# Kernel optimization log

Measured on AMD Instinct MI355X. Metric: run time of the kernel, lower is better.

Reference implementation:

```python
import jax, jax.numpy as jnp
import numpy as np

B, NQ, ISIZE = 8, 2048, 1024
H, D, NA = 8, 128, 8            # num_head, attn_dim, num_anchor
AH = H * D                      # ahsize = 1024
ASZ = NA * D                    # anchor_size = 1024
FH = 4096                       # _fhsize
ISZ_NET = FH * H // NA          # 4096, input dim of self.net
EPS = 1e-6


def setup_inputs() -> dict:
    key = jax.random.key(0)
    ks = jax.random.split(key, 12)
    def u(k, shape, fan_in):
        s = 1.0 / np.sqrt(fan_in)
        return jax.random.uniform(k, shape, jnp.float32, -s, s)
    return {
        "inputs": jax.random.normal(ks[0], (B, NQ, ISIZE), jnp.float32),
        "ln_g": jnp.ones((ISIZE,), jnp.float32),
        "ln_b": jnp.zeros((ISIZE,), jnp.float32),
        "q_anchor": u(ks[1], (H, NA, D), D),
        "W_qkv": u(ks[2], (ISIZE, 3 * AH), ISIZE), "b_qkv": jnp.zeros((3 * AH,), jnp.float32),
        "W_an": u(ks[3], (ASZ, FH), ASZ), "b_an": jnp.zeros((FH,), jnp.float32),
        "W_n1": u(ks[4], (ISZ_NET, AH), ISZ_NET), "b_n1": jnp.zeros((AH,), jnp.float32),
        "W_n2": u(ks[5], (AH, FH), AH), "b_n2": jnp.zeros((FH,), jnp.float32),
        "W_n3": u(ks[6], (FH, AH), FH), "b_n3": jnp.zeros((AH,), jnp.float32),
        "W_k": u(ks[7], (AH, AH), AH), "b_k": jnp.zeros((AH,), jnp.float32),
        "W_o": u(ks[8], (AH, ISIZE), AH), "b_o": jnp.zeros((ISIZE,), jnp.float32),
    }


def reference(inputs, ln_g, ln_b, q_anchor, W_qkv, b_qkv, W_an, b_an,
              W_n1, b_n1, W_n2, b_n2, W_n3, b_n3, W_k, b_k, W_o, b_o):
    b, nq = inputs.shape[:2]
    scale = 1.0 / np.sqrt(D)
    # pre-LayerNorm
    mu = jnp.mean(inputs, -1, keepdims=True)
    var = jnp.mean(jnp.square(inputs - mu), -1, keepdims=True)
    x = (inputs - mu) * jax.lax.rsqrt(var + EPS) * ln_g + ln_b
    # QKV projection
    qkv = (x @ W_qkv + b_qkv).reshape(b, nq, 3, H, D)
    q = jnp.transpose(qkv[:, :, 0], (0, 2, 1, 3))   # [b,H,nq,D]
    k = qkv[:, :, 1]                                  # [b,nq,H,D]
    v = qkv[:, :, 2]                                  # [b,nq,H,D]
    # stage 1: fixed anchors attend over the sequence
    sc1 = jax.nn.softmax(jnp.einsum('had,bnhd->bhan', q_anchor, k) * scale, axis=-1)
    out = jnp.einsum('bhan,bnhd->bhad', sc1, v).reshape(b, H, ASZ)   # [b,H,NA*D]
    # anchor_net (share_head Linear + ReLU)
    out = jax.nn.relu(out @ W_an + b_an)                              # [b,H,FH]
    # regroup head-major -> anchor-major
    out = out.reshape(b, H, NA, FH // NA).transpose(0, 2, 1, 3).reshape(b, NA, ISZ_NET)
    # net: bottleneck Linear -> Linear -> ReLU -> Linear
    out = jax.nn.relu((out @ W_n1 + b_n1) @ W_n2 + b_n2) @ W_n3 + b_n3  # [b,NA,AH]
    # stage 2: queries attend over anchors
    kk = (out @ W_k + b_k).reshape(b, NA, H, D)
    sc2 = jax.nn.softmax(jnp.einsum('bhqd,bahd->bhqa', q, kk) * scale, axis=-1)
    ov = out.reshape(b, NA, H, D)
    y = jnp.einsum('bhqa,bahd->bqhd', sc2, ov).reshape(b, nq, AH)
    return y @ W_o + b_o + inputs
```

## Files before the change

### kernel.cpp

```cpp
#include <hip/hip_runtime.h>
#include <cstdint>
#include <cstddef>

typedef unsigned short u16;
typedef __attribute__((ext_vector_type(8))) short short8;
typedef __attribute__((ext_vector_type(4))) float floatx4;
typedef __attribute__((ext_vector_type(16))) float floatx16;

__device__ __forceinline__ u16 f2bf(float f) {
  unsigned u = __float_as_uint(f);
  u += 0x7fffu + ((u >> 16) & 1u);
  return (u16)(u >> 16);
}
__device__ __forceinline__ float bf2f(u16 s) {
  return __uint_as_float(((unsigned)s) << 16);
}

__global__ __launch_bounds__(256) void ln_kernel(const float* __restrict__ x,
                                                 const float* __restrict__ g,
                                                 const float* __restrict__ bta,
                                                 u16* __restrict__ out) {
  const int row = blockIdx.x;
  const int tid = threadIdx.x;
  const float4 v = ((const float4*)(x + (size_t)row * 1024))[tid];
  float s = v.x + v.y + v.z + v.w;
#pragma unroll
  for (int o = 32; o > 0; o >>= 1) s += __shfl_down(s, o);
  __shared__ float red[4], red2[4];
  const int wv = tid >> 6, ln = tid & 63;
  if (ln == 0) red[wv] = s;
  __syncthreads();
  const float mean = (red[0] + red[1] + red[2] + red[3]) * (1.0f / 1024.0f);
  const float dx = v.x - mean, dy = v.y - mean, dz = v.z - mean, dw = v.w - mean;
  float s2 = dx * dx + dy * dy + dz * dz + dw * dw;
#pragma unroll
  for (int o = 32; o > 0; o >>= 1) s2 += __shfl_down(s2, o);
  if (ln == 0) red2[wv] = s2;
  __syncthreads();
  const float var = (red2[0] + red2[1] + red2[2] + red2[3]) * (1.0f / 1024.0f);
  const float rstd = rsqrtf(var + 1e-6f);
  const float4 gg = ((const float4*)g)[tid];
  const float4 bb = ((const float4*)bta)[tid];
  ushort4 o4;
  o4.x = f2bf(dx * rstd * gg.x + bb.x);
  o4.y = f2bf(dy * rstd * gg.y + bb.y);
  o4.z = f2bf(dz * rstd * gg.z + bb.z);
  o4.w = f2bf(dw * rstd * gg.w + bb.w);
  ((ushort4*)(out + (size_t)row * 1024))[tid] = o4;
}

__global__ __launch_bounds__(256) void transpose2_bf16(const float* __restrict__ Wq,
                                                       u16* __restrict__ WqT,
                                                       const float* __restrict__ Wo,
                                                       u16* __restrict__ WoT) {
  __shared__ float t[32][33];
  const float* W;
  u16* WT;
  int N, yb;
  if (blockIdx.y < 96) { W = Wq; WT = WqT; N = 3072; yb = blockIdx.y; }
  else { W = Wo; WT = WoT; N = 1024; yb = blockIdx.y - 96; }
  const int kb = blockIdx.x * 32, nb = yb * 32;
  const int tx = threadIdx.x & 31, ty = threadIdx.x >> 5;
#pragma unroll
  for (int i = ty; i < 32; i += 8) t[i][tx] = W[(size_t)(kb + i) * N + nb + tx];
  __syncthreads();
#pragma unroll
  for (int i = ty; i < 32; i += 8) WT[(size_t)(nb + i) * 1024 + kb + tx] = f2bf(t[tx][i]);
}

__global__ __launch_bounds__(256) void init_bufs(const float* __restrict__ b_an,
                                                 const float* __restrict__ b_n1,
                                                 const float* __restrict__ b_n2,
                                                 const float* __restrict__ b_n3,
                                                 const float* __restrict__ b_k,
                                                 float* __restrict__ att1,
                                                 float* __restrict__ anp,
                                                 float* __restrict__ h1,
                                                 float* __restrict__ h2,
                                                 float* __restrict__ onet,
                                                 float* __restrict__ kkb) {
  const int i = blockIdx.x * 256 + threadIdx.x;
  if (i < 16384) {
    float4 z; z.x = 0.f; z.y = 0.f; z.z = 0.f; z.w = 0.f;
    ((float4*)att1)[i] = z;
  } else if (i < 81920) {
    const int j = i - 16384;
    ((float4*)anp)[j] = ((const float4*)b_an)[j & 1023];
  } else if (i < 98304) {
    const int j = i - 81920;
    ((float4*)h1)[j] = ((const float4*)b_n1)[j & 255];
  } else if (i < 163840) {
    const int j = i - 98304;
    ((float4*)h2)[j] = ((const float4*)b_n2)[j & 1023];
  } else if (i < 180224) {
    const int j = i - 163840;
    ((float4*)onet)[j] = ((const float4*)b_n3)[j & 255];
  } else {
    const int j = i - 180224;
    ((float4*)kkb)[j] = ((const float4*)b_k)[j & 255];
  }
}


__device__ __forceinline__ void stageG(const u16* __restrict__ gp, u16* lp, int K) {
  __builtin_amdgcn_global_load_lds((const __attribute__((address_space(1))) void*)gp,
                                   (__attribute__((address_space(3))) void*)lp, 16, 0, 0);
  __builtin_amdgcn_global_load_lds((const __attribute__((address_space(1))) void*)(gp + ((size_t)K << 6)),
                                   (__attribute__((address_space(3))) void*)(lp + 4096), 16, 0, 0);
}

__device__ __forceinline__ void rdA(short8 (&af)[2][4], const u16* sbuf, const int (&ab)[4],
                                    int halfoff) {
#pragma unroll
  for (int mi = 0; mi < 2; ++mi)
#pragma unroll
    for (int ks = 0; ks < 4; ++ks)
      af[mi][ks] = *(const short8*)(sbuf + halfoff + mi * 2048 + (ab[ks] ^ (mi << 5)));
}
__device__ __forceinline__ void rdB(short8 (&bf)[4], const u16* sbuf, const int (&bb)[4],
                                    int halfoff) {
#pragma unroll
  for (int ks = 0; ks < 4; ++ks)
    bf[ks] = *(const short8*)(sbuf + halfoff + bb[ks]);
}

template <int Q>
__device__ __forceinline__ void mfmaQ(floatx16 (&acc)[4][2], const short8 (&af)[2][4],
                                      const short8 (&bf)[4]) {
#pragma unroll
  for (int ks = 0; ks < 4; ++ks)
#pragma unroll
    for (int mi = 0; mi < 2; ++mi)
      acc[Q][mi] = __builtin_amdgcn_mfma_f32_32x32x16_bf16(af[mi][ks], bf[ks], acc[Q][mi], 0, 0, 0);
}

template <int B_>
__device__ __forceinline__ void gtile(int t, int NT, int K,
                                      u16 (&sA)[2][16384], u16 (&sB)[2][16384],
                                      const u16* gA_lo, const u16* gA_hi,
                                      const u16* gB_lo, const u16* gB_hi,
                                      u16* ldsA_cur, u16* ldsA_alt,
                                      u16* ldsB_cur, u16* ldsB_alt,
                                      const int (&ab)[4], const int (&bb)[4],
                                      floatx16 (&acc)[4][2],
                                      short8 (&afA)[2][4], short8 (&bfP)[4], short8 (&bfN)[4]) {
  rdA(afA, sA[B_], ab, 0);
  __builtin_amdgcn_sched_barrier(0);
  if (t + 1 < NT) stageG(gA_hi + ((t + 1) << 6), ldsA_alt + 8192, K);
  rdB(bfN, sB[B_], bb, 8192);
  asm volatile("s_waitcnt lgkmcnt(4)" ::: "memory");
  __builtin_amdgcn_sched_barrier(0);
  __builtin_amdgcn_s_setprio(1);
  mfmaQ<0>(acc, afA, bfP);
  __builtin_amdgcn_s_setprio(0);
  if (t + 1 < NT) stageG(gB_lo + ((t + 1) << 6), ldsB_alt, K);
  asm volatile("s_waitcnt lgkmcnt(0)" ::: "memory");
  __builtin_amdgcn_sched_barrier(0);
  __builtin_amdgcn_s_setprio(1);
  mfmaQ<1>(acc, afA, bfN);
  __builtin_amdgcn_s_setprio(0);
  rdA(afA, sA[B_], ab, 8192);
  __builtin_amdgcn_s_barrier();
  if (t + 2 < NT) stageG(gA_lo + ((t + 2) << 6), ldsA_cur, K);
  asm volatile("s_waitcnt lgkmcnt(0)" ::: "memory");
  __builtin_amdgcn_sched_barrier(0);
  __builtin_amdgcn_s_setprio(1);
  mfmaQ<2>(acc, afA, bfN);
  __builtin_amdgcn_s_setprio(0);
  if (t + 2 < NT) stageG(gB_hi + ((t + 2) << 6), ldsB_cur + 8192, K);
  if (t + 2 < NT) {
    asm volatile("s_waitcnt vmcnt(4)" ::: "memory");
  } else {
    asm volatile("s_waitcnt vmcnt(0)" ::: "memory");
  }
  __builtin_amdgcn_s_barrier();
  if (t + 1 < NT) rdB(bfN, sB[B_ ^ 1], bb, 0);
  __builtin_amdgcn_sched_barrier(0);
  __builtin_amdgcn_s_setprio(1);
  mfmaQ<3>(acc, afA, bfP);
  __builtin_amdgcn_s_setprio(0);
}

template <int EPI>
__global__ __launch_bounds__(512, 2) void gemm_bf16(const u16* __restrict__ A,
                                                    const u16* __restrict__ BT,
                                                    const float* __restrict__ bias,
                                                    const float* __restrict__ extra,
                                                    u16* __restrict__ outB,
                                                    float* __restrict__ outF,
                                                    int M, int N, int K) {
  __shared__ u16 sA[2][16384];
  __shared__ u16 sB[2][16384];
  const int tid = threadIdx.x;
  const int wave = tid >> 6, lane = tid & 63;
  const int m0 = blockIdx.x * 256, n0 = blockIdx.y * 256;
  const int wr = wave >> 2, wc = wave & 3;
  const int l31 = lane & 31, l5 = lane >> 5, l7 = lane & 7;
  const int NT = K >> 6;

  const int fa = l7 ^ (l31 >> 3);
  const int fb = l7 ^ ((wc * 4 + (l31 >> 3)) & 7);
  int ab[4], bb[4];
#pragma unroll
  for (int ks = 0; ks < 4; ++ks) {
    const int kg = (ks << 1) + l5;
    ab[ks] = (wr * 64 + l31) * 64 + (((kg ^ fa) & 7) << 3);
    bb[ks] = (wc * 32 + l31) * 64 + (((kg ^ fb) & 7) << 3);
  }
  const int srow = wave * 8 + (lane >> 3);
  const int scol = ((lane & 7) ^ (lane >> 3) ^ wave) << 3;
  const u16* gA_lo = A + (size_t)(m0 + srow) * K + scol;
  const u16* gA_hi = A + (size_t)(m0 + 128 + srow) * K + scol;
  const u16* gB_lo = BT + (size_t)(n0 + srow) * K + scol;
  const u16* gB_hi = BT + (size_t)(n0 + 128 + srow) * K + scol;

  floatx16 acc[4][2];
#pragma unroll
  for (int q = 0; q < 4; ++q)
#pragma unroll
    for (int mi = 0; mi < 2; ++mi)
#pragma unroll
      for (int r = 0; r < 16; ++r) acc[q][mi][r] = 0.f;

  stageG(gA_lo, &sA[0][0] + wave * 512, K);
  stageG(gA_hi, &sA[0][8192] + wave * 512, K);
  stageG(gB_lo, &sB[0][0] + wave * 512, K);
  stageG(gB_hi, &sB[0][8192] + wave * 512, K);
  stageG(gA_lo + 64, &sA[1][0] + wave * 512, K);
  stageG(gB_hi + 64, &sB[1][8192] + wave * 512, K);
  asm volatile("s_waitcnt vmcnt(4)" ::: "memory");
  __builtin_amdgcn_s_barrier();

  short8 afA[2][4], bfX[4], bfY[4];
  rdB(bfX, sB[0], bb, 0);
  __builtin_amdgcn_sched_barrier(0);

  for (int t = 0; t < NT; t += 2) {
    gtile<0>(t, NT, K, sA, sB, gA_lo, gA_hi, gB_lo, gB_hi,
             &sA[0][0] + wave * 512, &sA[1][0] + wave * 512,
             &sB[0][0] + wave * 512, &sB[1][0] + wave * 512, ab, bb, acc, afA, bfX, bfY);
    gtile<1>(t + 1, NT, K, sA, sB, gA_lo, gA_hi, gB_lo, gB_hi,
             &sA[1][0] + wave * 512, &sA[0][0] + wave * 512,
             &sB[1][0] + wave * 512, &sB[0][0] + wave * 512, ab, bb, acc, afA, bfY, bfX);
  }

#pragma unroll
  for (int q = 0; q < 4; ++q) {
    const int QM = q >> 1, QN = QM ^ (q & 1);
    const int n = n0 + QN * 128 + wc * 32 + l31;
    const float bs = bias[n];
#pragma unroll
    for (int mi = 0; mi < 2; ++mi) {
      const int mb = m0 + QM * 128 + wr * 64 + mi * 32 + 4 * l5;
#pragma unroll
      for (int reg = 0; reg < 16; ++reg) {
        const int m = mb + (reg & 3) + 8 * (reg >> 2);
        const float v = acc[q][mi][reg] + bs;
        if (EPI == 0)
          outB[(size_t)m * N + n] = f2bf(v);
        else
          outF[(size_t)m * N + n] = v + extra[(size_t)m * N + n];
      }
    }
  }
}

__global__ __launch_bounds__(256) void attn1_scores(const u16* __restrict__ qkv,
                                                    const float* __restrict__ q_anchor,
                                                    float* __restrict__ S) {
  __shared__ float qa[8][128];
  const int tid = threadIdx.x;
  const int chunk = blockIdx.x & 7, bh = blockIdx.x >> 3;
  const int b = bh >> 3, h = bh & 7;
  for (int i = tid; i < 1024; i += 256) qa[i >> 7][i & 127] = q_anchor[h * 1024 + i];
  __syncthreads();
  const float scale = 0.0883883476483184f;
  const int n = chunk * 256 + tid;
  const u16* kp = qkv + (size_t)(b * 2048 + n) * 3072 + 1024 + h * 128;
  float dots[8] = {0, 0, 0, 0, 0, 0, 0, 0};
#pragma unroll 8
  for (int dd = 0; dd < 128; dd += 4) {
    const ushort4 k4 = *(const ushort4*)(kp + dd);
    const float k0 = bf2f(k4.x), k1 = bf2f(k4.y), k2 = bf2f(k4.z), k3 = bf2f(k4.w);
#pragma unroll
    for (int a = 0; a < 8; ++a) {
      const float4 q4 = *(const float4*)&qa[a][dd];
      dots[a] += q4.x * k0 + q4.y * k1 + q4.z * k2 + q4.w * k3;
    }
  }
#pragma unroll
  for (int a = 0; a < 8; ++a) S[((size_t)(bh * 8 + a)) * 2048 + n] = dots[a] * scale;
}

__global__ __launch_bounds__(256) void attn1_softmax(float* __restrict__ S) {
  const int row = blockIdx.x;
  const int tid = threadIdx.x;
  float* Sp = S + (size_t)row * 2048;
  float4 v0 = ((const float4*)Sp)[tid * 2];
  float4 v1 = ((const float4*)Sp)[tid * 2 + 1];
  float mx = fmaxf(fmaxf(fmaxf(v0.x, v0.y), fmaxf(v0.z, v0.w)),
                   fmaxf(fmaxf(v1.x, v1.y), fmaxf(v1.z, v1.w)));
#pragma unroll
  for (int o = 32; o > 0; o >>= 1) mx = fmaxf(mx, __shfl_xor(mx, o));
  __shared__ float red[4];
  const int wv = tid >> 6, ln = tid & 63;
  if (ln == 0) red[wv] = mx;
  __syncthreads();
  mx = fmaxf(fmaxf(red[0], red[1]), fmaxf(red[2], red[3]));
  v0.x = __expf(v0.x - mx); v0.y = __expf(v0.y - mx);
  v0.z = __expf(v0.z - mx); v0.w = __expf(v0.w - mx);
  v1.x = __expf(v1.x - mx); v1.y = __expf(v1.y - mx);
  v1.z = __expf(v1.z - mx); v1.w = __expf(v1.w - mx);
  float sum = v0.x + v0.y + v0.z + v0.w + v1.x + v1.y + v1.z + v1.w;
#pragma unroll
  for (int o = 32; o > 0; o >>= 1) sum += __shfl_xor(sum, o);
  __shared__ float red2[4];
  if (ln == 0) red2[wv] = sum;
  __syncthreads();
  const float inv = 1.f / (red2[0] + red2[1] + red2[2] + red2[3]);
  v0.x *= inv; v0.y *= inv; v0.z *= inv; v0.w *= inv;
  v1.x *= inv; v1.y *= inv; v1.z *= inv; v1.w *= inv;
  ((float4*)Sp)[tid * 2] = v0;
  ((float4*)Sp)[tid * 2 + 1] = v1;
}

__global__ __launch_bounds__(256) void attn1_pv(const u16* __restrict__ qkv,
                                                const float* __restrict__ S,
                                                float* __restrict__ att1) {
  __shared__ float P[8][256];
  const int tid = threadIdx.x;
  const int chunk = blockIdx.x & 7, bh = blockIdx.x >> 3;
  const int b = bh >> 3, h = bh & 7;
  for (int i = tid; i < 2048; i += 256) {
    const int a = i >> 8, n = i & 255;
    P[a][n] = S[((size_t)(bh * 8 + a)) * 2048 + chunk * 256 + n];
  }
  __syncthreads();
  const int d = tid & 127, half = tid >> 7;
  const int nbase = chunk * 256 + half * 128;
  const u16* vp = qkv + (size_t)(b * 2048 + nbase) * 3072 + 2048 + h * 128 + d;
  float acc[8] = {0.f};
  for (int n = 0; n < 128; n += 4) {
    const float v0 = bf2f(vp[(size_t)n * 3072]);
    const float v1 = bf2f(vp[(size_t)(n + 1) * 3072]);
    const float v2 = bf2f(vp[(size_t)(n + 2) * 3072]);
    const float v3 = bf2f(vp[(size_t)(n + 3) * 3072]);
#pragma unroll
    for (int a = 0; a < 8; ++a) {
      const float4 s4 = *(const float4*)&P[a][half * 128 + n];
      acc[a] += s4.x * v0 + s4.y * v1 + s4.z * v2 + s4.w * v3;
    }
  }
#pragma unroll
  for (int a = 0; a < 8; ++a)
    atomicAdd(&att1[(size_t)bh * 1024 + a * 128 + d], acc[a]);
}

template <int AMODE>
__global__ __launch_bounds__(256) void mlp_mfma(const float* __restrict__ A,
                                                const float* __restrict__ W,
                                                float* __restrict__ outp,
                                                int K, int N, int KC) {
  __shared__ float sW[64][33];
  const int tid = threadIdx.x;
  const int lane = tid & 63, wave = tid >> 6;
  const int wm = wave * 16;
  const int n0 = blockIdx.x * 64;
  const int kbeg = blockIdx.y * KC;
  const int l15 = lane & 15, kq8 = (lane >> 4) * 8;
  const int arow = wm + l15;

  floatx4 acc[4];
  const floatx4 zero = {0.f, 0.f, 0.f, 0.f};
#pragma unroll
  for (int j = 0; j < 4; ++j) acc[j] = zero;

  for (int kc = 0; kc < KC; kc += 32) {
    const int kbase = kbeg + kc;
    __syncthreads();
#pragma unroll
    for (int p = 0; p < 8; ++p) {
      const int k = p * 4 + wave;
      sW[lane][k] = W[(size_t)(kbase + k) * N + n0 + lane];
    }
    const float* ap;
    if (AMODE == 2) {
      const int k = kbase + kq8;
      ap = A + (size_t)(arow >> 3) * 32768 + (size_t)(k >> 9) * 4096 + (arow & 7) * 512 + (k & 511);
    } else {
      ap = A + (size_t)arow * K + kbase + kq8;
    }
    float4 a0 = *(const float4*)ap;
    float4 a1 = *(const float4*)(ap + 4);
    if (AMODE >= 1) {
      a0.x = fmaxf(a0.x, 0.f); a0.y = fmaxf(a0.y, 0.f);
      a0.z = fmaxf(a0.z, 0.f); a0.w = fmaxf(a0.w, 0.f);
      a1.x = fmaxf(a1.x, 0.f); a1.y = fmaxf(a1.y, 0.f);
      a1.z = fmaxf(a1.z, 0.f); a1.w = fmaxf(a1.w, 0.f);
    }
    short8 af;
    af[0] = (short)f2bf(a0.x); af[1] = (short)f2bf(a0.y);
    af[2] = (short)f2bf(a0.z); af[3] = (short)f2bf(a0.w);
    af[4] = (short)f2bf(a1.x); af[5] = (short)f2bf(a1.y);
    af[6] = (short)f2bf(a1.z); af[7] = (short)f2bf(a1.w);
    __syncthreads();
#pragma unroll
    for (int j = 0; j < 4; ++j) {
      const float* wp = &sW[j * 16 + l15][kq8];
      short8 bf;
      bf[0] = (short)f2bf(wp[0]); bf[1] = (short)f2bf(wp[1]);
      bf[2] = (short)f2bf(wp[2]); bf[3] = (short)f2bf(wp[3]);
      bf[4] = (short)f2bf(wp[4]); bf[5] = (short)f2bf(wp[5]);
      bf[6] = (short)f2bf(wp[6]); bf[7] = (short)f2bf(wp[7]);
      acc[j] = __builtin_amdgcn_mfma_f32_16x16x32_bf16(af, bf, acc[j], 0, 0, 0);
    }
  }
  const int q = lane >> 4;
#pragma unroll
  for (int j = 0; j < 4; ++j)
#pragma unroll
    for (int r = 0; r < 4; ++r) {
      const int m = wm + q * 4 + r;
      const int n = n0 + j * 16 + l15;
      atomicAdd(&outp[(size_t)m * N + n], acc[j][r]);
    }
}

__global__ __launch_bounds__(256) void attn2_kernel(const u16* __restrict__ qkv,
                                                    const float* __restrict__ kk,
                                                    const float* __restrict__ onet,
                                                    u16* __restrict__ y) {
  __shared__ float kkl[8][128];
  __shared__ float ovl[8][128];
  const int tid = threadIdx.x;
  const int chunk = blockIdx.x & 7, bh = blockIdx.x >> 3;
  const int b = bh >> 3, h = bh & 7;
  for (int i = tid; i < 1024; i += 256) {
    const int a = i >> 7, d = i & 127;
    kkl[a][d] = kk[(size_t)(b * 8 + a) * 1024 + h * 128 + d];
    ovl[a][d] = onet[(size_t)(b * 8 + a) * 1024 + h * 128 + d];
  }
  __syncthreads();
  const int n = chunk * 256 + tid;
  const u16* qp = qkv + (size_t)(b * 2048 + n) * 3072 + h * 128;
  float dots[8] = {0, 0, 0, 0, 0, 0, 0, 0};
#pragma unroll 4
  for (int dd = 0; dd < 128; dd += 4) {
    const ushort4 q4 = *(const ushort4*)(qp + dd);
    const float q0 = bf2f(q4.x), q1 = bf2f(q4.y), q2 = bf2f(q4.z), q3 = bf2f(q4.w);
#pragma unroll
    for (int a = 0; a < 8; ++a) {
      const float4 k4 = *(const float4*)&kkl[a][dd];
      dots[a] += k4.x * q0 + k4.y * q1 + k4.z * q2 + k4.w * q3;
    }
  }
  const float scale = 0.0883883476483184f;
  float mx = -1e30f;
#pragma unroll
  for (int a = 0; a < 8; ++a) {
    dots[a] *= scale;
    mx = fmaxf(mx, dots[a]);
  }
  float p[8];
  float sum = 0.f;
#pragma unroll
  for (int a = 0; a < 8; ++a) {
    p[a] = __expf(dots[a] - mx);
    sum += p[a];
  }
  const float inv = 1.f / sum;
#pragma unroll
  for (int a = 0; a < 8; ++a) p[a] *= inv;
  u16* yp = y + (size_t)(b * 2048 + n) * 1024 + h * 128;
#pragma unroll 4
  for (int dd = 0; dd < 128; dd += 4) {
    float a0 = 0, a1 = 0, a2 = 0, a3 = 0;
#pragma unroll
    for (int a = 0; a < 8; ++a) {
      const float4 o4 = *(const float4*)&ovl[a][dd];
      a0 += p[a] * o4.x;
      a1 += p[a] * o4.y;
      a2 += p[a] * o4.z;
      a3 += p[a] * o4.w;
    }
    ushort4 o;
    o.x = f2bf(a0);
    o.y = f2bf(a1);
    o.z = f2bf(a2);
    o.w = f2bf(a3);
    *(ushort4*)(yp + dd) = o;
  }
}

extern "C" void kernel_launch(void* const* d_in, const int* in_sizes, int n_in,
                              void* d_out, int out_size, void* d_ws, size_t ws_size,
                              hipStream_t stream) {
  const float* inputs = (const float*)d_in[0];
  const float* ln_g = (const float*)d_in[1];
  const float* ln_b = (const float*)d_in[2];
  const float* q_anchor = (const float*)d_in[3];
  const float* W_qkv = (const float*)d_in[4];
  const float* b_qkv = (const float*)d_in[5];
  const float* W_an = (const float*)d_in[6];
  const float* b_an = (const float*)d_in[7];
  const float* W_n1 = (const float*)d_in[8];
  const float* b_n1 = (const float*)d_in[9];
  const float* W_n2 = (const float*)d_in[10];
  const float* b_n2 = (const float*)d_in[11];
  const float* W_n3 = (const float*)d_in[12];
  const float* b_n3 = (const float*)d_in[13];
  const float* W_k = (const float*)d_in[14];
  const float* b_k = (const float*)d_in[15];
  const float* W_o = (const float*)d_in[16];
  const float* b_o = (const float*)d_in[17];
  float* out = (float*)d_out;

  char* ws = (char*)d_ws;
  u16* qkv = (u16*)(ws);
  u16* xbf = (u16*)(ws + 100663296);
  float* S = (float*)(ws + 100663296);
  u16* WqkvT = (u16*)(ws + 134217728);
  u16* WoT = (u16*)(ws + 140509184);
  float* att1 = (float*)(ws + 142606336);
  float* anp = (float*)(ws + 142868480);
  float* h1 = (float*)(ws + 143917056);
  float* h2 = (float*)(ws + 144179200);
  float* onet = (float*)(ws + 145227776);
  float* kkb = (float*)(ws + 145489920);

  ln_kernel<<<16384, 256, 0, stream>>>(inputs, ln_g, ln_b, xbf);
  transpose2_bf16<<<dim3(32, 128), 256, 0, stream>>>(W_qkv, WqkvT, W_o, WoT);
  init_bufs<<<768, 256, 0, stream>>>(b_an, b_n1, b_n2, b_n3, b_k,
                                     att1, anp, h1, h2, onet, kkb);
  gemm_bf16<0><<<dim3(64, 12), 512, 0, stream>>>(xbf, WqkvT, b_qkv, nullptr, qkv, nullptr,
                                                 16384, 3072, 1024);
  attn1_scores<<<512, 256, 0, stream>>>(qkv, q_anchor, S);
  attn1_softmax<<<512, 256, 0, stream>>>(S);
  attn1_pv<<<512, 256, 0, stream>>>(qkv, S, att1);
  mlp_mfma<0><<<dim3(64, 4), 256, 0, stream>>>(att1, W_an, anp, 1024, 4096, 256);
  mlp_mfma<2><<<dim3(16, 16), 256, 0, stream>>>(anp, W_n1, h1, 4096, 1024, 256);
  mlp_mfma<0><<<dim3(64, 4), 256, 0, stream>>>(h1, W_n2, h2, 1024, 4096, 256);
  mlp_mfma<1><<<dim3(16, 16), 256, 0, stream>>>(h2, W_n3, onet, 4096, 1024, 256);
  mlp_mfma<0><<<dim3(16, 8), 256, 0, stream>>>(onet, W_k, kkb, 1024, 1024, 128);
  attn2_kernel<<<512, 256, 0, stream>>>(qkv, kkb, onet, xbf);
  gemm_bf16<1><<<dim3(64, 4), 512, 0, stream>>>(xbf, WoT, b_o, inputs, nullptr, out,
                                                16384, 1024, 1024);
}
```

Before: 578.1 us.

## Fuse anchor attention stages into one kernel and merge prep kernels

Merges layernorm, weight transpose and bias-init into a single prep launch. It also replaces the three-kernel stage-1 anchor attention (scores, softmax, PV with atomics) with one fused kernel that stages K/V tiles in shared memory, keeps scores in LDS, and writes normalized outputs directly. This removes the S buffer round trip, the att1 zeroing and the atomics. The cost is fewer blocks (256) that each re-read K and V four times, once per anchor pair, plus heavy LDS use that may limit occupancy.

```diff
diff --git a/kernel.cpp b/kernel.cpp
--- a/kernel.cpp
+++ b/kernel.cpp
@@ -16,88 +16,86 @@
   return __uint_as_float(((unsigned)s) << 16);
 }
 
-__global__ __launch_bounds__(256) void ln_kernel(const float* __restrict__ x,
-                                                 const float* __restrict__ g,
-                                                 const float* __restrict__ bta,
-                                                 u16* __restrict__ out) {
-  const int row = blockIdx.x;
+__global__ __launch_bounds__(256) void prep_kernel(const float* __restrict__ x,
+                                                   const float* __restrict__ g,
+                                                   const float* __restrict__ bta,
+                                                   u16* __restrict__ xout,
+                                                   const float* __restrict__ Wq,
+                                                   u16* __restrict__ WqT,
+                                                   const float* __restrict__ Wo,
+                                                   u16* __restrict__ WoT,
+                                                   const float* __restrict__ b_an,
+                                                   const float* __restrict__ b_n1,
+                                                   const float* __restrict__ b_n2,
+                                                   const float* __restrict__ b_n3,
+                                                   const float* __restrict__ b_k,
+                                                   float* __restrict__ anp,
+                                                   float* __restrict__ h1,
+                                                   float* __restrict__ h2,
+                                                   float* __restrict__ onet,
+                                                   float* __restrict__ kkb) {
+  __shared__ float t[32][33];
+  __shared__ float red[4], red2[4];
+  const int bid = blockIdx.x;
   const int tid = threadIdx.x;
-  const float4 v = ((const float4*)(x + (size_t)row * 1024))[tid];
-  float s = v.x + v.y + v.z + v.w;
-#pragma unroll
-  for (int o = 32; o > 0; o >>= 1) s += __shfl_down(s, o);
-  __shared__ float red[4], red2[4];
-  const int wv = tid >> 6, ln = tid & 63;
-  if (ln == 0) red[wv] = s;
-  __syncthreads();
-  const float mean = (red[0] + red[1] + red[2] + red[3]) * (1.0f / 1024.0f);
-  const float dx = v.x - mean, dy = v.y - mean, dz = v.z - mean, dw = v.w - mean;
-  float s2 = dx * dx + dy * dy + dz * dz + dw * dw;
-#pragma unroll
-  for (int o = 32; o > 0; o >>= 1) s2 += __shfl_down(s2, o);
-  if (ln == 0) red2[wv] = s2;
-  __syncthreads();
-  const float var = (red2[0] + red2[1] + red2[2] + red2[3]) * (1.0f / 1024.0f);
-  const float rstd = rsqrtf(var + 1e-6f);
-  const float4 gg = ((const float4*)g)[tid];
-  const float4 bb = ((const float4*)bta)[tid];
-  ushort4 o4;
-  o4.x = f2bf(dx * rstd * gg.x + bb.x);
-  o4.y = f2bf(dy * rstd * gg.y + bb.y);
-  o4.z = f2bf(dz * rstd * gg.z + bb.z);
-  o4.w = f2bf(dw * rstd * gg.w + bb.w);
-  ((ushort4*)(out + (size_t)row * 1024))[tid] = o4;
-}
-
-__global__ __launch_bounds__(256) void transpose2_bf16(const float* __restrict__ Wq,
-                                                       u16* __restrict__ WqT,
-                                                       const float* __restrict__ Wo,
-                                                       u16* __restrict__ WoT) {
-  __shared__ float t[32][33];
-  const float* W;
-  u16* WT;
-  int N, yb;
-  if (blockIdx.y < 96) { W = Wq; WT = WqT; N = 3072; yb = blockIdx.y; }
-  else { W = Wo; WT = WoT; N = 1024; yb = blockIdx.y - 96; }
-  const int kb = blockIdx.x * 32, nb = yb * 32;
-  const int tx = threadIdx.x & 31, ty = threadIdx.x >> 5;
-#pragma unroll
-  for (int i = ty; i < 32; i += 8) t[i][tx] = W[(size_t)(kb + i) * N + nb + tx];
-  __syncthreads();
-#pragma unroll
-  for (int i = ty; i < 32; i += 8) WT[(size_t)(nb + i) * 1024 + kb + tx] = f2bf(t[tx][i]);
-}
-
-__global__ __launch_bounds__(256) void init_bufs(const float* __restrict__ b_an,
-                                                 const float* __restrict__ b_n1,
-                                                 const float* __restrict__ b_n2,
-                                                 const float* __restrict__ b_n3,
-                                                 const float* __restrict__ b_k,
-                                                 float* __restrict__ att1,
-                                                 float* __restrict__ anp,
-                                                 float* __restrict__ h1,
-                                                 float* __restrict__ h2,
-                                                 float* __restrict__ onet,
-                                                 float* __restrict__ kkb) {
-  const int i = blockIdx.x * 256 + threadIdx.x;
-  if (i < 16384) {
-    float4 z; z.x = 0.f; z.y = 0.f; z.z = 0.f; z.w = 0.f;
-    ((float4*)att1)[i] = z;
-  } else if (i < 81920) {
-    const int j = i - 16384;
-    ((float4*)anp)[j] = ((const float4*)b_an)[j & 1023];
-  } else if (i < 98304) {
-    const int j = i - 81920;
-    ((float4*)h1)[j] = ((const float4*)b_n1)[j & 255];
-  } else if (i < 163840) {
-    const int j = i - 98304;
-    ((float4*)h2)[j] = ((const float4*)b_n2)[j & 1023];
-  } else if (i < 180224) {
-    const int j = i - 163840;
-    ((float4*)onet)[j] = ((const float4*)b_n3)[j & 255];
+  if (bid < 16384) {
+    const int row = bid;
+    const float4 v = ((const float4*)(x + (size_t)row * 1024))[tid];
+    float s = v.x + v.y + v.z + v.w;
+#pragma unroll
+    for (int o = 32; o > 0; o >>= 1) s += __shfl_down(s, o);
+    const int wv = tid >> 6, ln = tid & 63;
+    if (ln == 0) red[wv] = s;
+    __syncthreads();
+    const float mean = (red[0] + red[1] + red[2] + red[3]) * (1.0f / 1024.0f);
+    const float dx = v.x - mean, dy = v.y - mean, dz = v.z - mean, dw = v.w - mean;
+    float s2 = dx * dx + dy * dy + dz * dz + dw * dw;
+#pragma unroll
+    for (int o = 32; o > 0; o >>= 1) s2 += __shfl_down(s2, o);
+    if (ln == 0) red2[wv] = s2;
+    __syncthreads();
+    const float var = (red2[0] + red2[1] + red2[2] + red2[3]) * (1.0f / 1024.0f);
+    const float rstd = rsqrtf(var + 1e-6f);
+    const float4 gg = ((const float4*)g)[tid];
+    const float4 bb = ((const float4*)bta)[tid];
+    ushort4 o4;
+    o4.x = f2bf(dx * rstd * gg.x + bb.x);
+    o4.y = f2bf(dy * rstd * gg.y + bb.y);
+    o4.z = f2bf(dz * rstd * gg.z + bb.z);
+    o4.w = f2bf(dw * rstd * gg.w + bb.w);
+    ((ushort4*)(xout + (size_t)row * 1024))[tid] = o4;
+  } else if (bid < 20480) {
+    const int t2 = bid - 16384;
+    const int xb = t2 & 31, yb0 = t2 >> 5;
+    const float* W;
+    u16* WT;
+    int N, yb;
+    if (yb0 < 96) { W = Wq; WT = WqT; N = 3072; yb = yb0; }
+    else { W = Wo; WT = WoT; N = 1024; yb = yb0 - 96; }
+    const int kb = xb * 32, nb = yb * 32;
+    const int tx = tid & 31, ty = tid >> 5;
+#pragma unroll
+    for (int i = ty; i < 32; i += 8) t[i][tx] = W[(size_t)(kb + i) * N + nb + tx];
+    __syncthreads();
+#pragma unroll
+    for (int i = ty; i < 32; i += 8) WT[(size_t)(nb + i) * 1024 + kb + tx] = f2bf(t[tx][i]);
   } else {
-    const int j = i - 180224;
-    ((float4*)kkb)[j] = ((const float4*)b_k)[j & 255];
+    const int i = (bid - 20480) * 256 + tid;
+    if (i < 65536) {
+      ((float4*)anp)[i] = ((const float4*)b_an)[i & 1023];
+    } else if (i < 81920) {
+      const int j = i - 65536;
+      ((float4*)h1)[j] = ((const float4*)b_n1)[j & 255];
+    } else if (i < 147456) {
+      const int j = i - 81920;
+      ((float4*)h2)[j] = ((const float4*)b_n2)[j & 1023];
+    } else if (i < 163840) {
+      const int j = i - 147456;
+      ((float4*)onet)[j] = ((const float4*)b_n3)[j & 255];
+    } else {
+      const int j = i - 163840;
+      ((float4*)kkb)[j] = ((const float4*)b_k)[j & 255];
+    }
   }
 }
 
@@ -265,95 +263,111 @@
   }
 }
 
-__global__ __launch_bounds__(256) void attn1_scores(const u16* __restrict__ qkv,
-                                                    const float* __restrict__ q_anchor,
-                                                    float* __restrict__ S) {
-  __shared__ float qa[8][128];
+__global__ __launch_bounds__(512) void attn1_fused(const u16* __restrict__ qkv,
+                                                   const float* __restrict__ q_anchor,
+                                                   float* __restrict__ att1) {
+  __shared__ u16 kv[256 * 132];
+  __shared__ float S2[2][2048];
+  __shared__ float qa2[2][128];
+  __shared__ float red[16];
   const int tid = threadIdx.x;
-  const int chunk = blockIdx.x & 7, bh = blockIdx.x >> 3;
+  const int bh = blockIdx.x >> 2, ag = blockIdx.x & 3;
   const int b = bh >> 3, h = bh & 7;
-  for (int i = tid; i < 1024; i += 256) qa[i >> 7][i & 127] = q_anchor[h * 1024 + i];
+  const int a0 = ag * 2;
+
+  for (int i = tid; i < 256; i += 512)
+    qa2[i >> 7][i & 127] = q_anchor[h * 1024 + (a0 + (i >> 7)) * 128 + (i & 127)];
+
+  const float scale = 0.0883883476483184f;
+  const size_t rowbase = (size_t)b * 2048;
+
+  {
+    const int a = tid >> 8, nn = tid & 255;
+    for (int T = 0; T < 8; ++T) {
+      __syncthreads();
+#pragma unroll
+      for (int p = 0; p < 16; ++p) {
+        const int c = p * 512 + tid;
+        const int r = c >> 5, off = (c & 31) * 4;
+        const ushort4 kk = *(const ushort4*)(qkv + (rowbase + T * 256 + r) * 3072 + 1024 + h * 128 + off);
+        *(ushort4*)&kv[r * 132 + off] = kk;
+      }
+      __syncthreads();
+      float dot = 0.f;
+#pragma unroll 8
+      for (int dd = 0; dd < 128; dd += 4) {
+        const ushort4 k4 = *(const ushort4*)&kv[nn * 132 + dd];
+        const float4 q4 = *(const float4*)&qa2[a][dd];
+        dot += q4.x * bf2f(k4.x) + q4.y * bf2f(k4.y) + q4.z * bf2f(k4.z) + q4.w * bf2f(k4.w);
+      }
+      S2[a][T * 256 + nn] = dot * scale;
+    }
+  }
   __syncthreads();
-  const float scale = 0.0883883476483184f;
-  const int n = chunk * 256 + tid;
-  const u16* kp = qkv + (size_t)(b * 2048 + n) * 3072 + 1024 + h * 128;
-  float dots[8] = {0, 0, 0, 0, 0, 0, 0, 0};
-#pragma unroll 8
-  for (int dd = 0; dd < 128; dd += 4) {
-    const ushort4 k4 = *(const ushort4*)(kp + dd);
-    const float k0 = bf2f(k4.x), k1 = bf2f(k4.y), k2 = bf2f(k4.z), k3 = bf2f(k4.w);
-#pragma unroll
-    for (int a = 0; a < 8; ++a) {
-      const float4 q4 = *(const float4*)&qa[a][dd];
-      dots[a] += q4.x * k0 + q4.y * k1 + q4.z * k2 + q4.w * k3;
-    }
-  }
-#pragma unroll
-  for (int a = 0; a < 8; ++a) S[((size_t)(bh * 8 + a)) * 2048 + n] = dots[a] * scale;
-}
-
-__global__ __launch_bounds__(256) void attn1_softmax(float* __restrict__ S) {
-  const int row = blockIdx.x;
-  const int tid = threadIdx.x;
-  float* Sp = S + (size_t)row * 2048;
-  float4 v0 = ((const float4*)Sp)[tid * 2];
-  float4 v1 = ((const float4*)Sp)[tid * 2 + 1];
-  float mx = fmaxf(fmaxf(fmaxf(v0.x, v0.y), fmaxf(v0.z, v0.w)),
-                   fmaxf(fmaxf(v1.x, v1.y), fmaxf(v1.z, v1.w)));
-#pragma unroll
-  for (int o = 32; o > 0; o >>= 1) mx = fmaxf(mx, __shfl_xor(mx, o));
-  __shared__ float red[4];
-  const int wv = tid >> 6, ln = tid & 63;
-  if (ln == 0) red[wv] = mx;
+  {
+    const int a = tid >> 8, li = tid & 255;
+    const int wv = (tid >> 6) & 3, ln = tid & 63;
+    float mx = -1e30f;
+#pragma unroll
+    for (int k = 0; k < 8; ++k) mx = fmaxf(mx, S2[a][li + k * 256]);
+#pragma unroll
+    for (int o = 32; o > 0; o >>= 1) mx = fmaxf(mx, __shfl_xor(mx, o));
+    if (ln == 0) red[a * 4 + wv] = mx;
+    __syncthreads();
+    mx = fmaxf(fmaxf(red[a * 4], red[a * 4 + 1]), fmaxf(red[a * 4 + 2], red[a * 4 + 3]));
+    float sum = 0.f;
+#pragma unroll
+    for (int k = 0; k < 8; ++k) {
+      const float e = __expf(S2[a][li + k * 256] - mx);
+      S2[a][li + k * 256] = e;
+      sum += e;
+    }
+#pragma unroll
+    for (int o = 32; o > 0; o >>= 1) sum += __shfl_xor(sum, o);
+    if (ln == 0) red[8 + a * 4 + wv] = sum;
+  }
   __syncthreads();
-  mx = fmaxf(fmaxf(red[0], red[1]), fmaxf(red[2], red[3]));
-  v0.x = __expf(v0.x - mx); v0.y = __expf(v0.y - mx);
-  v0.z = __expf(v0.z - mx); v0.w = __expf(v0.w - mx);
-  v1.x = __expf(v1.x - mx); v1.y = __expf(v1.y - mx);
-  v1.z = __expf(v1.z - mx); v1.w = __expf(v1.w - mx);
-  float sum = v0.x + v0.y + v0.z + v0.w + v1.x + v1.y + v1.z + v1.w;
-#pragma unroll
-  for (int o = 32; o > 0; o >>= 1) sum += __shfl_xor(sum, o);
-  __shared__ float red2[4];
-  if (ln == 0) red2[wv] = sum;
+  {
+    const int a2 = tid & 1, dq = (tid >> 1) & 31, s = tid >> 6;
+    float acc0 = 0.f, acc1 = 0.f, acc2 = 0.f, acc3 = 0.f;
+    for (int T = 0; T < 8; ++T) {
+      __syncthreads();
+#pragma unroll
+      for (int p = 0; p < 16; ++p) {
+        const int c = p * 512 + tid;
+        const int r = c >> 5, off = (c & 31) * 4;
+        const ushort4 vv = *(const ushort4*)(qkv + (rowbase + T * 256 + r) * 3072 + 2048 + h * 128 + off);
+        *(ushort4*)&kv[r * 132 + off] = vv;
+      }
+      __syncthreads();
+#pragma unroll 4
+      for (int j = 0; j < 32; ++j) {
+        const int nl = s * 32 + j;
+        const float pw = S2[a2][T * 256 + nl];
+        const ushort4 v4 = *(const ushort4*)&kv[nl * 132 + dq * 4];
+        acc0 += pw * bf2f(v4.x);
+        acc1 += pw * bf2f(v4.y);
+        acc2 += pw * bf2f(v4.z);
+        acc3 += pw * bf2f(v4.w);
+      }
+    }
+    __syncthreads();
+    float* scratch = &S2[0][0];
+    scratch[((a2 * 32 + dq) * 4 + 0) * 8 + s] = acc0;
+    scratch[((a2 * 32 + dq) * 4 + 1) * 8 + s] = acc1;
+    scratch[((a2 * 32 + dq) * 4 + 2) * 8 + s] = acc2;
+    scratch[((a2 * 32 + dq) * 4 + 3) * 8 + s] = acc3;
+  }
   __syncthreads();
-  const float inv = 1.f / (red2[0] + red2[1] + red2[2] + red2[3]);
-  v0.x *= inv; v0.y *= inv; v0.z *= inv; v0.w *= inv;
-  v1.x *= inv; v1.y *= inv; v1.z *= inv; v1.w *= inv;
-  ((float4*)Sp)[tid * 2] = v0;
-  ((float4*)Sp)[tid * 2 + 1] = v1;
-}
-
-__global__ __launch_bounds__(256) void attn1_pv(const u16* __restrict__ qkv,
-                                                const float* __restrict__ S,
-                                                float* __restrict__ att1) {
-  __shared__ float P[8][256];
-  const int tid = threadIdx.x;
-  const int chunk = blockIdx.x & 7, bh = blockIdx.x >> 3;
-  const int b = bh >> 3, h = bh & 7;
-  for (int i = tid; i < 2048; i += 256) {
-    const int a = i >> 8, n = i & 255;
-    P[a][n] = S[((size_t)(bh * 8 + a)) * 2048 + chunk * 256 + n];
-  }
-  __syncthreads();
-  const int d = tid & 127, half = tid >> 7;
-  const int nbase = chunk * 256 + half * 128;
-  const u16* vp = qkv + (size_t)(b * 2048 + nbase) * 3072 + 2048 + h * 128 + d;
-  float acc[8] = {0.f};
-  for (int n = 0; n < 128; n += 4) {
-    const float v0 = bf2f(vp[(size_t)n * 3072]);
-    const float v1 = bf2f(vp[(size_t)(n + 1) * 3072]);
-    const float v2 = bf2f(vp[(size_t)(n + 2) * 3072]);
-    const float v3 = bf2f(vp[(size_t)(n + 3) * 3072]);
-#pragma unroll
-    for (int a = 0; a < 8; ++a) {
-      const float4 s4 = *(const float4*)&P[a][half * 128 + n];
-      acc[a] += s4.x * v0 + s4.y * v1 + s4.z * v2 + s4.w * v3;
-    }
-  }
-#pragma unroll
-  for (int a = 0; a < 8; ++a)
-    atomicAdd(&att1[(size_t)bh * 1024 + a * 128 + d], acc[a]);
+  if (tid < 256) {
+    const int a2 = tid >> 7, dq = (tid >> 2) & 31, k = tid & 3;
+    const float* scratch = &S2[0][0];
+    const float* sp = &scratch[((a2 * 32 + dq) * 4 + k) * 8];
+    float tot = sp[0] + sp[1] + sp[2] + sp[3] + sp[4] + sp[5] + sp[6] + sp[7];
+    const float inv = 1.f / (red[8 + a2 * 4] + red[8 + a2 * 4 + 1] +
+                             red[8 + a2 * 4 + 2] + red[8 + a2 * 4 + 3]);
+    att1[(size_t)bh * 1024 + (a0 + a2) * 128 + dq * 4 + k] = tot * inv;
+  }
 }
 
 template <int AMODE>
@@ -518,7 +532,6 @@
   char* ws = (char*)d_ws;
   u16* qkv = (u16*)(ws);
   u16* xbf = (u16*)(ws + 100663296);
-  float* S = (float*)(ws + 100663296);
   u16* WqkvT = (u16*)(ws + 134217728);
   u16* WoT = (u16*)(ws + 140509184);
   float* att1 = (float*)(ws + 142606336);
@@ -528,15 +541,13 @@
   float* onet = (float*)(ws + 145227776);
   float* kkb = (float*)(ws + 145489920);
 
-  ln_kernel<<<16384, 256, 0, stream>>>(inputs, ln_g, ln_b, xbf);
-  transpose2_bf16<<<dim3(32, 128), 256, 0, stream>>>(W_qkv, WqkvT, W_o, WoT);
-  init_bufs<<<768, 256, 0, stream>>>(b_an, b_n1, b_n2, b_n3, b_k,
-                                     att1, anp, h1, h2, onet, kkb);
+  prep_kernel<<<21184, 256, 0, stream>>>(inputs, ln_g, ln_b, xbf,
+                                         W_qkv, WqkvT, W_o, WoT,
+                                         b_an, b_n1, b_n2, b_n3, b_k,
+                                         anp, h1, h2, onet, kkb);
   gemm_bf16<0><<<dim3(64, 12), 512, 0, stream>>>(xbf, WqkvT, b_qkv, nullptr, qkv, nullptr,
                                                  16384, 3072, 1024);
-  attn1_scores<<<512, 256, 0, stream>>>(qkv, q_anchor, S);
-  attn1_softmax<<<512, 256, 0, stream>>>(S);
-  attn1_pv<<<512, 256, 0, stream>>>(qkv, S, att1);
+  attn1_fused<<<256, 512, 0, stream>>>(qkv, q_anchor, att1);
   mlp_mfma<0><<<dim3(64, 4), 256, 0, stream>>>(att1, W_an, anp, 1024, 4096, 256);
   mlp_mfma<2><<<dim3(16, 16), 256, 0, stream>>>(anp, W_n1, h1, 4096, 1024, 256);
   mlp_mfma<0><<<dim3(64, 4), 256, 0, stream>>>(h1, W_n2, h2, 1024, 4096, 256);
```

Measured after the change: 574.7 us. About the same (-0.6%).
